# Performance work log

Measured on AMD Instinct MI355X. Metric: run time of the kernel, lower is better.

The kernel has to match this reference:

```python
import jax, jax.numpy as jnp
import numpy as np

NX = 1024
LENGTH = 0.1
BATCH = 16
COF = 0.25 * (LENGTH / (NX - 1)) ** 2  # 0.25 * STRIDE^2 / TEMPER_COEFFICIENT


def setup_inputs() -> dict:
    key = jax.random.key(0)
    k1, k2 = jax.random.split(key)
    layout = jax.random.uniform(k1, (BATCH, NX, NX, 1), dtype=jnp.float32)
    heat = jax.random.normal(k2, (BATCH, NX, NX, 1), dtype=jnp.float32)
    return {"layout": layout, "heat": heat, "n_iter": 50}


def _stencil(x):
    # reflect-pad then 3x3 cross stencil: 0.25*(up+down+left+right), NHWC
    xp = jnp.pad(x, ((0, 0), (1, 1), (1, 1), (0, 0)), mode="reflect")
    return 0.25 * (
        xp[:, :-2, 1:-1, :] + xp[:, 2:, 1:-1, :]
        + xp[:, 1:-1, :-2, :] + xp[:, 1:-1, 2:, :]
    )


def reference(layout, heat, n_iter):
    f = COF * layout
    G = jnp.ones_like(heat)  # bcs=None -> no Dirichlet mask zeros

    def body(i, x):
        return G * (_stencil(x) + f)

    x0 = heat * G
    return jax.lax.fori_loop(0, n_iter, body, x0)
```

## Files before the change

### kernel.cpp

```cpp
#include <hip/hip_runtime.h>


#define NX 1024
#define BATCH 16
#define OUTC 96
#define T16 16
#define PITCH 128
#define SLOTS 34

typedef float v2f __attribute__((ext_vector_type(2)));

__device__ __forceinline__ int reflect_idx(int i) {
    i = (i < 0) ? -i : i;
    return (i > NX - 1) ? 2 * (NX - 1) - i : i;
}

__device__ __forceinline__ float dpp_wshr1(float x) {
    int v = __float_as_int(x);
    return __int_as_float(__builtin_amdgcn_update_dpp(v, v, 0x138, 0xF, 0xF, false));
}
__device__ __forceinline__ float dpp_wshl1(float x) {
    int v = __float_as_int(x);
    return __int_as_float(__builtin_amdgcn_update_dpp(v, v, 0x130, 0xF, 0xF, false));
}

__device__ __forceinline__ v2f pk_add(v2f a, v2f b) {
    v2f d; asm("v_pk_add_f32 %0, %1, %2" : "=v"(d) : "v"(a), "v"(b)); return d;
}
__device__ __forceinline__ v2f pk_fma(v2f a, v2f b, v2f c) {
    v2f d; asm("v_pk_fma_f32 %0, %1, %2, %3" : "=v"(d) : "v"(a), "v"(b), "v"(c)); return d;
}

__device__ __forceinline__ void jrow(v2f uE, v2f uO, v2f cE, v2f cO,
                                     v2f dE, v2f dO, v2f fe, v2f fo,
                                     v2f qq, v2f& rE, v2f& rO) {
    v2f vE = pk_add(uE, dE);
    v2f vO = pk_add(uO, dO);
    v2f P; P.x = dpp_wshr1(cO.y); P.y = cO.x;
    v2f Q; Q.x = cE.y; Q.y = dpp_wshl1(cE.x);
    v2f hE = pk_add(P, cO);
    v2f hO = pk_add(cE, Q);
    rE = pk_fma(pk_add(vE, hE), qq, fe);
    rO = pk_fma(pk_add(vO, hO), qq, fo);
}

template<int T, int OUTR>
__global__ __launch_bounds__(512, 4) void jacobi_fused(const float* __restrict__ src,
                                                       const float* __restrict__ layout,
                                                       float* __restrict__ dst) {
    __shared__ float buf[2][SLOTS * PITCH];

    const float COF = (float)(0.25 * (0.1 / 1023.0) * (0.1 / 1023.0));

    const int tid = threadIdx.x;
    const int g = tid & 31;
    const int c = tid >> 5;
    const int gr0 = blockIdx.y * OUTR - T;
    const int gc0 = blockIdx.x * OUTC - T16;
    const int base = blockIdx.z * NX * NX;
    const int R0 = 1 + 8 * c;
    const int C0 = 4 * g;

    v2f E[8], O[8], fE[8], fO[8];

    const bool interior = (blockIdx.x >= 1) && (blockIdx.x <= 9) &&
                          (blockIdx.y >= 1) && (blockIdx.y <= 8);

    if (interior) {
        const float* sb = src + base + (gr0 + R0) * NX + gc0 + C0;
        const float* lb = layout + base + (gr0 + R0) * NX + gc0 + C0;
#pragma unroll
        for (int i = 0; i < 8; ++i) {
            float4 v = *(const float4*)(sb + i * NX);
            E[i] = (v2f){v.x, v.z};
            O[i] = (v2f){v.y, v.w};
        }
#pragma unroll
        for (int i = 0; i < 8; ++i) {
            float4 v = *(const float4*)(lb + i * NX);
            fE[i] = (v2f){COF * v.x, COF * v.z};
            fO[i] = (v2f){COF * v.y, COF * v.w};
        }
        if (tid < 128) {
            const int rsel = tid >> 6;
            const int q2 = tid & 63;
            const int slot = rsel ? 32 : 1;
            v2f v = *(const v2f*)(src + base + (gr0 + (rsel ? 129 : 0)) * NX + gc0 + 2 * q2);
            const int lo = 4 * (q2 >> 1) + (q2 & 1);
            buf[0][slot * PITCH + lo]     = v.x;
            buf[0][slot * PITCH + lo + 2] = v.y;
        }
    } else {
        const int c0 = reflect_idx(gc0 + C0);
        const int c1 = reflect_idx(gc0 + C0 + 1);
        const int c2 = reflect_idx(gc0 + C0 + 2);
        const int c3 = reflect_idx(gc0 + C0 + 3);
#pragma unroll
        for (int i = 0; i < 8; ++i) {
            const int grr = reflect_idx(gr0 + R0 + i);
            const float* sr = src + base + grr * NX;
            const float* lr = layout + base + grr * NX;
            E[i]  = (v2f){sr[c0], sr[c2]};
            O[i]  = (v2f){sr[c1], sr[c3]};
            fE[i] = (v2f){COF * lr[c0], COF * lr[c2]};
            fO[i] = (v2f){COF * lr[c1], COF * lr[c3]};
        }
        if (tid < 256) {
            const int rsel = tid >> 7;
            const int q = tid & 127;
            const int slot = rsel ? 32 : 1;
            const int grr = reflect_idx(gr0 + (rsel ? 129 : 0));
            const int lo = (q & ~3) | ((q & 1) << 1) | ((q >> 1) & 1);
            buf[0][slot * PITCH + lo] = src[base + grr * NX + reflect_idx(gc0 + q)];
        }
    }

    const v2f qq = (v2f){0.25f, 0.25f};
    const int wT = (2 * c) * PITCH + C0;
    const int wB = (2 * c + 3) * PITCH + C0;
    const int rT = (2 * c + 1) * PITCH + C0;
    const int rB = (2 * c + 2) * PITCH + C0;

    *(v2f*)&buf[0][wT]     = E[0];
    *(v2f*)&buf[0][wT + 2] = O[0];
    *(v2f*)&buf[0][wB]     = E[7];
    *(v2f*)&buf[0][wB + 2] = O[7];

#pragma unroll
    for (int s = 0; s < T; ++s) {
        __syncthreads();
        const float* rb = buf[s & 1];
        float* wb = buf[(s + 1) & 1];
        const float4 t  = *(const float4*)&rb[rT];
        const float4 bo = *(const float4*)&rb[rB];

        const v2f oE0 = E[0], oO0 = O[0], oE1 = E[1], oO1 = O[1];
        v2f upE = E[0], upO = O[0];

#pragma unroll
        for (int i = 1; i <= 3; ++i) {
            v2f sE = E[i], sO = O[i];
            jrow(upE, upO, sE, sO, E[i + 1], O[i + 1], fE[i], fO[i], qq, E[i], O[i]);
            upE = sE; upO = sO;
        }

        {
            v2f topE = (v2f){t.x, t.y}, topO = (v2f){t.z, t.w};
            jrow(topE, topO, oE0, oO0, oE1, oO1, fE[0], fO[0], qq, E[0], O[0]);
        }
        if (s + 1 < T) {
            *(v2f*)&wb[wT]     = E[0];
            *(v2f*)&wb[wT + 2] = O[0];
        }

#pragma unroll
        for (int i = 4; i <= 6; ++i) {
            v2f sE = E[i], sO = O[i];
            jrow(upE, upO, sE, sO, E[i + 1], O[i + 1], fE[i], fO[i], qq, E[i], O[i]);
            upE = sE; upO = sO;
        }

        {
            v2f botE = (v2f){bo.x, bo.y}, botO = (v2f){bo.z, bo.w};
            jrow(upE, upO, E[7], O[7], botE, botO, fE[7], fO[7], qq, E[7], O[7]);
        }
        if (s + 1 < T) {
            *(v2f*)&wb[wB]     = E[7];
            *(v2f*)&wb[wB + 2] = O[7];
        }
    }

    const bool ok0 = (C0 >= T16) && (C0 < T16 + OUTC) && (gc0 + C0 + 1 < NX);
    const bool ok1 = (C0 + 2 >= T16) && (C0 + 2 < T16 + OUTC) && (gc0 + C0 + 3 < NX);
#pragma unroll
    for (int i = 0; i < 8; ++i) {
        const int br = R0 + i;
        const bool rowok = (br >= T) && (br <= 129 - T) && (gr0 + br < NX);
        if (rowok && ok0)
            *(v2f*)(dst + base + (gr0 + br) * NX + gc0 + C0) = (v2f){E[i].x, O[i].x};
        if (rowok && ok1)
            *(v2f*)(dst + base + (gr0 + br) * NX + gc0 + C0 + 2) = (v2f){E[i].y, O[i].y};
    }
}

extern "C" void kernel_launch(void* const* d_in, const int* in_sizes, int n_in,
                              void* d_out, int out_size, void* d_ws, size_t ws_size,
                              hipStream_t stream) {
    const float* layout = (const float*)d_in[0];
    const float* heat   = (const float*)d_in[1];
    float* out = (float*)d_out;
    float* ws  = (float*)d_ws;

    const dim3 g13(11, 10, BATCH), g11(11, 10, BATCH);
    const dim3 block(512);

    jacobi_fused<13, 104><<<g13, block, 0, stream>>>(heat, layout, ws);
    jacobi_fused<13, 104><<<g13, block, 0, stream>>>(ws,   layout, out);
    jacobi_fused<13, 104><<<g13, block, 0, stream>>>(out,  layout, ws);
    jacobi_fused<11, 108><<<g11, block, 0, stream>>>(ws,   layout, out);
}
```

Baseline: 374.4 us.

## Make Jacobi kernel persistent and prefetch next tile's patch during compute

Replaces the 3D grid of one-tile blocks with a persistent grid of 512 blocks that loop over all tiles. While computing the current tile's time steps, each block prefetches the next tile's source patch into registers, hiding global load latency behind the stencil sweep. It also swaps __syncthreads for a barrier that waits only on LDS counters, so in-flight global prefetches are not drained at every step. The risks are higher register pressure from the extra float4 buffer, and load imbalance because 1760 tiles do not divide evenly over 512 blocks.

After: 440.5 us. +17.7%, slower.

```diff
diff --git a/kernel.cpp b/kernel.cpp
--- a/kernel.cpp
+++ b/kernel.cpp
@@ -3,10 +3,14 @@
 
 #define NX 1024
 #define BATCH 16
+#define GBX 11
+#define GBY 10
+#define NTILES (GBX * GBY * BATCH)
 #define OUTC 96
 #define T16 16
 #define PITCH 128
 #define SLOTS 34
+#define NBLOCKS 512
 
 typedef float v2f __attribute__((ext_vector_type(2)));
 
@@ -44,10 +48,36 @@
     rO = pk_fma(pk_add(vO, hO), qq, fo);
 }
 
+__device__ __forceinline__ void bar_lds() {
+    asm volatile("s_waitcnt lgkmcnt(0)" ::: "memory");
+    __builtin_amdgcn_s_barrier();
+    asm volatile("" ::: "memory");
+}
+
 template<int T, int OUTR>
-__global__ __launch_bounds__(512, 4) void jacobi_fused(const float* __restrict__ src,
-                                                       const float* __restrict__ layout,
-                                                       float* __restrict__ dst) {
+__device__ __forceinline__ void load_patch(const float* __restrict__ src, int t,
+                                           int R0, int C0, float4 (&s4)[8]) {
+    const int bx = t % GBX, rem = t / GBX, by = rem % GBY, bz = rem / GBY;
+    const int gr0 = by * OUTR - T, gc0 = bx * OUTC - T16, base = bz * NX * NX;
+    if (bx >= 1 && bx <= 9 && by >= 1 && by <= 8) {
+        const float* sb = src + base + (gr0 + R0) * NX + gc0 + C0;
+#pragma unroll
+        for (int i = 0; i < 8; ++i) s4[i] = *(const float4*)(sb + i * NX);
+    } else {
+        const int c0 = reflect_idx(gc0 + C0), c1 = reflect_idx(gc0 + C0 + 1);
+        const int c2 = reflect_idx(gc0 + C0 + 2), c3 = reflect_idx(gc0 + C0 + 3);
+#pragma unroll
+        for (int i = 0; i < 8; ++i) {
+            const float* sr = src + base + reflect_idx(gr0 + R0 + i) * NX;
+            s4[i] = make_float4(sr[c0], sr[c1], sr[c2], sr[c3]);
+        }
+    }
+}
+
+template<int T, int OUTR>
+__global__ __launch_bounds__(512, 4) void jacobi_ms(const float* __restrict__ src,
+                                                    const float* __restrict__ layout,
+                                                    float* __restrict__ dst) {
     __shared__ float buf[2][SLOTS * PITCH];
 
     const float COF = (float)(0.25 * (0.1 / 1023.0) * (0.1 / 1023.0));
@@ -55,131 +85,125 @@
     const int tid = threadIdx.x;
     const int g = tid & 31;
     const int c = tid >> 5;
-    const int gr0 = blockIdx.y * OUTR - T;
-    const int gc0 = blockIdx.x * OUTC - T16;
-    const int base = blockIdx.z * NX * NX;
     const int R0 = 1 + 8 * c;
     const int C0 = 4 * g;
-
-    v2f E[8], O[8], fE[8], fO[8];
-
-    const bool interior = (blockIdx.x >= 1) && (blockIdx.x <= 9) &&
-                          (blockIdx.y >= 1) && (blockIdx.y <= 8);
-
-    if (interior) {
-        const float* sb = src + base + (gr0 + R0) * NX + gc0 + C0;
-        const float* lb = layout + base + (gr0 + R0) * NX + gc0 + C0;
-#pragma unroll
-        for (int i = 0; i < 8; ++i) {
-            float4 v = *(const float4*)(sb + i * NX);
-            E[i] = (v2f){v.x, v.z};
-            O[i] = (v2f){v.y, v.w};
-        }
-#pragma unroll
-        for (int i = 0; i < 8; ++i) {
-            float4 v = *(const float4*)(lb + i * NX);
-            fE[i] = (v2f){COF * v.x, COF * v.z};
-            fO[i] = (v2f){COF * v.y, COF * v.w};
-        }
-        if (tid < 128) {
-            const int rsel = tid >> 6;
-            const int q2 = tid & 63;
-            const int slot = rsel ? 32 : 1;
-            v2f v = *(const v2f*)(src + base + (gr0 + (rsel ? 129 : 0)) * NX + gc0 + 2 * q2);
-            const int lo = 4 * (q2 >> 1) + (q2 & 1);
-            buf[0][slot * PITCH + lo]     = v.x;
-            buf[0][slot * PITCH + lo + 2] = v.y;
-        }
-    } else {
-        const int c0 = reflect_idx(gc0 + C0);
-        const int c1 = reflect_idx(gc0 + C0 + 1);
-        const int c2 = reflect_idx(gc0 + C0 + 2);
-        const int c3 = reflect_idx(gc0 + C0 + 3);
-#pragma unroll
-        for (int i = 0; i < 8; ++i) {
-            const int grr = reflect_idx(gr0 + R0 + i);
-            const float* sr = src + base + grr * NX;
-            const float* lr = layout + base + grr * NX;
-            E[i]  = (v2f){sr[c0], sr[c2]};
-            O[i]  = (v2f){sr[c1], sr[c3]};
-            fE[i] = (v2f){COF * lr[c0], COF * lr[c2]};
-            fO[i] = (v2f){COF * lr[c1], COF * lr[c3]};
-        }
-        if (tid < 256) {
-            const int rsel = tid >> 7;
-            const int q = tid & 127;
-            const int slot = rsel ? 32 : 1;
-            const int grr = reflect_idx(gr0 + (rsel ? 129 : 0));
-            const int lo = (q & ~3) | ((q & 1) << 1) | ((q >> 1) & 1);
-            buf[0][slot * PITCH + lo] = src[base + grr * NX + reflect_idx(gc0 + q)];
-        }
-    }
-
     const v2f qq = (v2f){0.25f, 0.25f};
     const int wT = (2 * c) * PITCH + C0;
     const int wB = (2 * c + 3) * PITCH + C0;
     const int rT = (2 * c + 1) * PITCH + C0;
     const int rB = (2 * c + 2) * PITCH + C0;
 
-    *(v2f*)&buf[0][wT]     = E[0];
-    *(v2f*)&buf[0][wT + 2] = O[0];
-    *(v2f*)&buf[0][wB]     = E[7];
-    *(v2f*)&buf[0][wB + 2] = O[7];
-
-#pragma unroll
-    for (int s = 0; s < T; ++s) {
+    float4 s4[8];
+    load_patch<T, OUTR>(src, blockIdx.x, R0, C0, s4);
+
+#pragma unroll 1
+    for (int t = blockIdx.x; t < NTILES; t += NBLOCKS) {
+        const int bx = t % GBX, rem = t / GBX, by = rem % GBY, bz = rem / GBY;
+        const int gr0 = by * OUTR - T, gc0 = bx * OUTC - T16, base = bz * NX * NX;
+        const bool interior = (bx >= 1 && bx <= 9 && by >= 1 && by <= 8);
+
         __syncthreads();
-        const float* rb = buf[s & 1];
-        float* wb = buf[(s + 1) & 1];
-        const float4 t  = *(const float4*)&rb[rT];
-        const float4 bo = *(const float4*)&rb[rB];
-
-        const v2f oE0 = E[0], oO0 = O[0], oE1 = E[1], oO1 = O[1];
-        v2f upE = E[0], upO = O[0];
-
-#pragma unroll
-        for (int i = 1; i <= 3; ++i) {
-            v2f sE = E[i], sO = O[i];
-            jrow(upE, upO, sE, sO, E[i + 1], O[i + 1], fE[i], fO[i], qq, E[i], O[i]);
-            upE = sE; upO = sO;
-        }
-
-        {
-            v2f topE = (v2f){t.x, t.y}, topO = (v2f){t.z, t.w};
-            jrow(topE, topO, oE0, oO0, oE1, oO1, fE[0], fO[0], qq, E[0], O[0]);
-        }
-        if (s + 1 < T) {
-            *(v2f*)&wb[wT]     = E[0];
-            *(v2f*)&wb[wT + 2] = O[0];
-        }
-
-#pragma unroll
-        for (int i = 4; i <= 6; ++i) {
-            v2f sE = E[i], sO = O[i];
-            jrow(upE, upO, sE, sO, E[i + 1], O[i + 1], fE[i], fO[i], qq, E[i], O[i]);
-            upE = sE; upO = sO;
-        }
-
-        {
-            v2f botE = (v2f){bo.x, bo.y}, botO = (v2f){bo.z, bo.w};
-            jrow(upE, upO, E[7], O[7], botE, botO, fE[7], fO[7], qq, E[7], O[7]);
-        }
-        if (s + 1 < T) {
-            *(v2f*)&wb[wB]     = E[7];
-            *(v2f*)&wb[wB + 2] = O[7];
-        }
-    }
-
-    const bool ok0 = (C0 >= T16) && (C0 < T16 + OUTC) && (gc0 + C0 + 1 < NX);
-    const bool ok1 = (C0 + 2 >= T16) && (C0 + 2 < T16 + OUTC) && (gc0 + C0 + 3 < NX);
-#pragma unroll
-    for (int i = 0; i < 8; ++i) {
-        const int br = R0 + i;
-        const bool rowok = (br >= T) && (br <= 129 - T) && (gr0 + br < NX);
-        if (rowok && ok0)
-            *(v2f*)(dst + base + (gr0 + br) * NX + gc0 + C0) = (v2f){E[i].x, O[i].x};
-        if (rowok && ok1)
-            *(v2f*)(dst + base + (gr0 + br) * NX + gc0 + C0 + 2) = (v2f){E[i].y, O[i].y};
+
+        v2f E[8], O[8], fE[8], fO[8];
+#pragma unroll
+        for (int i = 0; i < 8; ++i) {
+            E[i] = (v2f){s4[i].x, s4[i].z};
+            O[i] = (v2f){s4[i].y, s4[i].w};
+        }
+
+        if (interior) {
+            const float* lb = layout + base + (gr0 + R0) * NX + gc0 + C0;
+#pragma unroll
+            for (int i = 0; i < 8; ++i) {
+                float4 v = *(const float4*)(lb + i * NX);
+                fE[i] = (v2f){COF * v.x, COF * v.z};
+                fO[i] = (v2f){COF * v.y, COF * v.w};
+            }
+            if (tid < 128) {
+                const int rsel = tid >> 6, q2 = tid & 63;
+                const int slot = rsel ? 32 : 1;
+                v2f v = *(const v2f*)(src + base + (gr0 + (rsel ? 129 : 0)) * NX + gc0 + 2 * q2);
+                const int lo = 4 * (q2 >> 1) + (q2 & 1);
+                buf[0][slot * PITCH + lo]     = v.x;
+                buf[0][slot * PITCH + lo + 2] = v.y;
+            }
+        } else {
+            const int c0 = reflect_idx(gc0 + C0), c1 = reflect_idx(gc0 + C0 + 1);
+            const int c2 = reflect_idx(gc0 + C0 + 2), c3 = reflect_idx(gc0 + C0 + 3);
+#pragma unroll
+            for (int i = 0; i < 8; ++i) {
+                const float* lr = layout + base + reflect_idx(gr0 + R0 + i) * NX;
+                fE[i] = (v2f){COF * lr[c0], COF * lr[c2]};
+                fO[i] = (v2f){COF * lr[c1], COF * lr[c3]};
+            }
+            if (tid < 256) {
+                const int rsel = tid >> 7, q = tid & 127;
+                const int slot = rsel ? 32 : 1;
+                const int grr = reflect_idx(gr0 + (rsel ? 129 : 0));
+                const int lo = (q & ~3) | ((q & 1) << 1) | ((q >> 1) & 1);
+                buf[0][slot * PITCH + lo] = src[base + grr * NX + reflect_idx(gc0 + q)];
+            }
+        }
+
+        *(v2f*)&buf[0][wT]     = E[0];
+        *(v2f*)&buf[0][wT + 2] = O[0];
+        *(v2f*)&buf[0][wB]     = E[7];
+        *(v2f*)&buf[0][wB + 2] = O[7];
+
+        if (t + NBLOCKS < NTILES)
+            load_patch<T, OUTR>(src, t + NBLOCKS, R0, C0, s4);
+
+#pragma unroll
+        for (int s = 0; s < T; ++s) {
+            bar_lds();
+            const float* rb = buf[s & 1];
+            float* wb = buf[(s + 1) & 1];
+            const float4 t4 = *(const float4*)&rb[rT];
+            const float4 b4 = *(const float4*)&rb[rB];
+
+            const v2f oE0 = E[0], oO0 = O[0], oE1 = E[1], oO1 = O[1];
+            v2f upE = E[0], upO = O[0];
+#pragma unroll
+            for (int i = 1; i <= 3; ++i) {
+                v2f sE = E[i], sO = O[i];
+                jrow(upE, upO, sE, sO, E[i + 1], O[i + 1], fE[i], fO[i], qq, E[i], O[i]);
+                upE = sE; upO = sO;
+            }
+            {
+                v2f topE = (v2f){t4.x, t4.y}, topO = (v2f){t4.z, t4.w};
+                jrow(topE, topO, oE0, oO0, oE1, oO1, fE[0], fO[0], qq, E[0], O[0]);
+            }
+            if (s + 1 < T) {
+                *(v2f*)&wb[wT]     = E[0];
+                *(v2f*)&wb[wT + 2] = O[0];
+            }
+#pragma unroll
+            for (int i = 4; i <= 6; ++i) {
+                v2f sE = E[i], sO = O[i];
+                jrow(upE, upO, sE, sO, E[i + 1], O[i + 1], fE[i], fO[i], qq, E[i], O[i]);
+                upE = sE; upO = sO;
+            }
+            {
+                v2f botE = (v2f){b4.x, b4.y}, botO = (v2f){b4.z, b4.w};
+                jrow(upE, upO, E[7], O[7], botE, botO, fE[7], fO[7], qq, E[7], O[7]);
+            }
+            if (s + 1 < T) {
+                *(v2f*)&wb[wB]     = E[7];
+                *(v2f*)&wb[wB + 2] = O[7];
+            }
+        }
+
+        const bool ok0 = (C0 >= T16) && (C0 < T16 + OUTC) && (gc0 + C0 + 1 < NX);
+        const bool ok1 = (C0 + 2 >= T16) && (C0 + 2 < T16 + OUTC) && (gc0 + C0 + 3 < NX);
+#pragma unroll
+        for (int i = 0; i < 8; ++i) {
+            const int br = R0 + i;
+            const bool rowok = (br >= T) && (br <= 129 - T) && (gr0 + br < NX);
+            if (rowok && ok0)
+                *(v2f*)(dst + base + (gr0 + br) * NX + gc0 + C0) = (v2f){E[i].x, O[i].x};
+            if (rowok && ok1)
+                *(v2f*)(dst + base + (gr0 + br) * NX + gc0 + C0 + 2) = (v2f){E[i].y, O[i].y};
+        }
     }
 }
 
@@ -191,11 +215,10 @@
     float* out = (float*)d_out;
     float* ws  = (float*)d_ws;
 
-    const dim3 g13(11, 10, BATCH), g11(11, 10, BATCH);
-    const dim3 block(512);
-
-    jacobi_fused<13, 104><<<g13, block, 0, stream>>>(heat, layout, ws);
-    jacobi_fused<13, 104><<<g13, block, 0, stream>>>(ws,   layout, out);
-    jacobi_fused<13, 104><<<g13, block, 0, stream>>>(out,  layout, ws);
-    jacobi_fused<11, 108><<<g11, block, 0, stream>>>(ws,   layout, out);
-}
+    const dim3 grid(NBLOCKS), block(512);
+
+    jacobi_ms<13, 104><<<grid, block, 0, stream>>>(heat, layout, ws);
+    jacobi_ms<13, 104><<<grid, block, 0, stream>>>(ws,   layout, out);
+    jacobi_ms<13, 104><<<grid, block, 0, stream>>>(out,  layout, ws);
+    jacobi_ms<11, 108><<<grid, block, 0, stream>>>(ws,   layout, out);
+}
```
